# Kernel tuning notes

Measured on AMD Instinct MI355X. Metric: run time of the kernel, lower is better.

Reference implementation:

```python
import jax, jax.numpy as jnp
import numpy as np

H, W = 128, 128
FOCAL_X = FOCAL_Y = 128.0
NEAR = 0.3
N_GAUSS = 2048
EPS = 1e-4  # regularizer on 2D covariance diagonal


def q2r(q):
    """Quaternion (w,x,y,z) [N,4] -> rotation matrices [N,3,3]."""
    q = q / jnp.linalg.norm(q, axis=-1, keepdims=True)
    w, x, y, z = q[:, 0], q[:, 1], q[:, 2], q[:, 3]
    R = jnp.stack([
        1 - 2 * (y * y + z * z), 2 * (x * y - w * z), 2 * (x * z + w * y),
        2 * (x * y + w * z), 1 - 2 * (x * x + z * z), 2 * (y * z - w * x),
        2 * (x * z - w * y), 2 * (y * z + w * x), 1 - 2 * (x * x + y * y),
    ], axis=-1).reshape(-1, 3, 3)
    return R


def setup_inputs():
    key = jax.random.key(0)
    ks = jax.random.split(key, 6)
    # gaussians placed inside the camera frustum (camera looks along +z)
    xy = jax.random.uniform(ks[0], (N_GAUSS, 2), minval=-1.5, maxval=1.5)
    z = jax.random.uniform(ks[1], (N_GAUSS, 1), minval=2.0, maxval=6.0)
    pos = jnp.concatenate([xy * z / 4.0, z], axis=-1)
    rgb = jax.random.normal(ks[2], (N_GAUSS, 3))
    opa = jax.random.normal(ks[3], (N_GAUSS,))
    quat = jax.random.normal(ks[4], (N_GAUSS, 4))
    scale = jax.random.uniform(ks[5], (N_GAUSS, 3), minval=0.01, maxval=0.05)
    ang = 0.05  # small camera rotation about y
    rot = jnp.array([[np.cos(ang), 0.0, np.sin(ang)],
                     [0.0, 1.0, 0.0],
                     [-np.sin(ang), 0.0, np.cos(ang)]], dtype=jnp.float32)
    tran = jnp.array([0.0, 0.0, 0.1], dtype=jnp.float32)
    return {"pos": pos, "rgb": rgb, "opa": opa, "quat": quat,
            "scale": scale, "rot": rot, "tran": tran}


def _forward(pos, rgb, opa, quat, scale, rot, tran):
    # ---- project: world -> camera -> image space (Gaussian3ds.project) ----
    pos_cam = pos @ rot.T + tran                       # [N,3]
    x, y, z = pos_cam[:, 0], pos_cam[:, 1], pos_cam[:, 2]
    r = jnp.linalg.norm(pos_cam, axis=-1)              # depth = ||p_cam||
    u, v = x / z, y / z                                # normalized image coords
    zero = jnp.zeros_like(z)
    # jacobian of (x/z, y/z, ||p||) wrt camera coords (jacobian_torch)
    J = jnp.stack([1.0 / z, zero, -x / (z * z),
                   zero, 1.0 / z, -y / (z * z),
                   x / r, y / r, z / r], axis=-1).reshape(-1, 3, 3)
    # 3D covariance: R S S^T R^T with abs scale activation
    Rm = q2r(quat)
    s = jnp.abs(scale) + 1e-4
    RS = Rm * s[:, None, :]                            # R @ diag(s)
    cov3d = jnp.einsum('nij,nkj->nik', RS, RS)
    JW = jnp.einsum('nij,jk->nik', J, rot)
    cov2d = jnp.einsum('nij,njk,nlk->nil', JW, cov3d, JW)[:, :2, :2]
    a = cov2d[:, 0, 0] + EPS
    b = cov2d[:, 0, 1]
    c = cov2d[:, 1, 1] + EPS
    det = a * c - b * b
    ia, ib, ic = c / det, -b / det, a / det            # inverse 2x2 cov entries
    rgb_s = jax.nn.sigmoid(rgb)
    opa_s = jax.nn.sigmoid(opa)
    # ---- global front-to-back depth sort ----
    order = jnp.argsort(r)
    u, v = u[order], v[order]
    ia, ib, ic = ia[order], ib[order], ic[order]
    opa_s, zs = opa_s[order], z[order]
    rgb_s = rgb_s[order]
    # ---- alpha composite over all pixels (tiles merged -> dense) ----
    px = (jnp.arange(W) - W / 2 + 0.5) / FOCAL_X
    py = (jnp.arange(H) - H / 2 + 0.5) / FOCAL_Y
    yy, xx = jnp.meshgrid(py, px, indexing='ij')
    pxf, pyf = xx.reshape(-1), yy.reshape(-1)          # [P]
    dx = pxf[:, None] - u[None, :]                     # [P,N]
    dy = pyf[:, None] - v[None, :]
    power = -0.5 * (ia * dx * dx + 2.0 * ib * dx * dy + ic * dy * dy)
    alpha = jnp.clip(opa_s * jnp.exp(power), 0.0, 0.99)
    alpha = alpha * (zs > NEAR)                        # near-plane cull as mask
    T = jnp.cumprod(1.0 - alpha, axis=1)
    T_excl = jnp.concatenate([jnp.ones((T.shape[0], 1), T.dtype), T[:, :-1]], axis=1)
    img = (T_excl * alpha) @ rgb_s                     # [P,3]
    return img.reshape(H, W, 3)


def reference(pos, rgb, opa, quat, scale, rot, tran):
    return _forward(pos, rgb, opa, quat, scale, rot, tran)
```

## Files before the change

### kernel.cpp

```cpp
#include <hip/hip_runtime.h>
#include <hip/hip_bf16.h>

#define NG     2048
#define HW     128
#define NPIX   (HW*HW)
#define SEG    16
#define CHUNK  (NG/SEG)
#define NEARZ  0.3f
#define GEPS   1e-4f
#define LOG2E  1.4426950408889634f

__device__ float4   g_ga_s[NG];
__device__ float4   g_gb_s[NG];
__device__ float    g_cb_s[NG];
__device__ unsigned g_bb_s[NG];

__device__ __forceinline__ float sigm(float x) { return 1.0f / (1.0f + __expf(-x)); }

__device__ __forceinline__ bool detect_f32(const void* rot) {
    return ((const unsigned short*)rot)[1] != 0;
}
__device__ __forceinline__ float ld(const void* p, int idx, bool f32) {
    if (f32) return ((const float*)p)[idx];
    return __bfloat162float(((const __hip_bfloat16*)p)[idx]);
}

__global__ __launch_bounds__(256)
void prep_sort_kernel(const void* __restrict__ pos,
                      const void* __restrict__ rgb,
                      const void* __restrict__ opa,
                      const void* __restrict__ quat,
                      const void* __restrict__ scale,
                      const void* __restrict__ rot,
                      const void* __restrict__ tran)
{
    __shared__ float rs[NG];
    __shared__ int   srank[16];

    int tid = threadIdx.x;
    bool f32 = detect_f32(rot);

    float R[9], T3[3];
    #pragma unroll
    for (int k = 0; k < 9; k++) R[k] = ld(rot, k, f32);
    #pragma unroll
    for (int k = 0; k < 3; k++) T3[k] = ld(tran, k, f32);

    #pragma unroll
    for (int k = 0; k < NG / 256; k++) {
        int j = tid + k * 256;
        float p0 = ld(pos, j*3+0, f32), p1 = ld(pos, j*3+1, f32), p2 = ld(pos, j*3+2, f32);
        float x = R[0]*p0 + R[1]*p1 + R[2]*p2 + T3[0];
        float y = R[3]*p0 + R[4]*p1 + R[5]*p2 + T3[1];
        float z = R[6]*p0 + R[7]*p1 + R[8]*p2 + T3[2];
        rs[j] = sqrtf(x*x + y*y + z*z);
    }
    __syncthreads();

    int g      = blockIdx.x * 16 + (tid >> 4);
    int lane16 = tid & 15;
    float ri = rs[g];
    int rank = 0;
    int jbase = lane16 * CHUNK;
    #pragma unroll 4
    for (int jj = 0; jj < CHUNK; jj++) {
        int j = jbase + ((jj + 2 * lane16) & (CHUNK - 1));
        float rj = rs[j];
        rank += (rj < ri) || (rj == ri && j < g);
    }
    #pragma unroll
    for (int d = 1; d < 16; d <<= 1) rank += __shfl_xor(rank, d);
    if (lane16 == 0) srank[tid >> 4] = rank;
    __syncthreads();

    if (tid < 16) {
        int i  = blockIdx.x * 16 + tid;
        int rk = srank[tid];

        float p0 = ld(pos, i*3+0, f32), p1 = ld(pos, i*3+1, f32), p2 = ld(pos, i*3+2, f32);
        float x = R[0]*p0 + R[1]*p1 + R[2]*p2 + T3[0];
        float y = R[3]*p0 + R[4]*p1 + R[5]*p2 + T3[1];
        float z = R[6]*p0 + R[7]*p1 + R[8]*p2 + T3[2];
        float iz = 1.0f / z;
        float u = x * iz, v = y * iz;

        float qw = ld(quat, i*4+0, f32), qx = ld(quat, i*4+1, f32);
        float qy = ld(quat, i*4+2, f32), qz = ld(quat, i*4+3, f32);
        float qn = 1.0f / sqrtf(qw*qw + qx*qx + qy*qy + qz*qz);
        qw *= qn; qx *= qn; qy *= qn; qz *= qn;
        float Rm[3][3];
        Rm[0][0] = 1.0f - 2.0f*(qy*qy + qz*qz);
        Rm[0][1] = 2.0f*(qx*qy - qw*qz);
        Rm[0][2] = 2.0f*(qx*qz + qw*qy);
        Rm[1][0] = 2.0f*(qx*qy + qw*qz);
        Rm[1][1] = 1.0f - 2.0f*(qx*qx + qz*qz);
        Rm[1][2] = 2.0f*(qy*qz - qw*qx);
        Rm[2][0] = 2.0f*(qx*qz - qw*qy);
        Rm[2][1] = 2.0f*(qy*qz + qw*qx);
        Rm[2][2] = 1.0f - 2.0f*(qx*qx + qy*qy);

        float s[3];
        #pragma unroll
        for (int k = 0; k < 3; k++) s[k] = fabsf(ld(scale, i*3+k, f32)) + 1e-4f;

        float RS[3][3];
        #pragma unroll
        for (int a = 0; a < 3; a++)
            #pragma unroll
            for (int b = 0; b < 3; b++) RS[a][b] = Rm[a][b] * s[b];
        float C3[3][3];
        #pragma unroll
        for (int a = 0; a < 3; a++)
            #pragma unroll
            for (int b = 0; b < 3; b++)
                C3[a][b] = RS[a][0]*RS[b][0] + RS[a][1]*RS[b][1] + RS[a][2]*RS[b][2];

        float nx = -x * iz * iz, ny = -y * iz * iz;
        float jw0[3], jw1[3];
        #pragma unroll
        for (int k = 0; k < 3; k++) {
            jw0[k] = iz * R[0*3+k] + nx * R[2*3+k];
            jw1[k] = iz * R[1*3+k] + ny * R[2*3+k];
        }
        float t0[3], t1[3];
        #pragma unroll
        for (int j = 0; j < 3; j++) {
            t0[j] = C3[j][0]*jw0[0] + C3[j][1]*jw0[1] + C3[j][2]*jw0[2];
            t1[j] = C3[j][0]*jw1[0] + C3[j][1]*jw1[1] + C3[j][2]*jw1[2];
        }
        float a = jw0[0]*t0[0] + jw0[1]*t0[1] + jw0[2]*t0[2] + GEPS;
        float b = jw0[0]*t1[0] + jw0[1]*t1[1] + jw0[2]*t1[2];
        float c = jw1[0]*t1[0] + jw1[1]*t1[1] + jw1[2]*t1[2] + GEPS;
        float det  = a*c - b*b;
        float idet = 1.0f / det;
        float Af = -0.5f * LOG2E * (c * idet);
        float Bf = -LOG2E * (-b * idet);
        float Cf = -0.5f * LOG2E * (a * idet);

        float om = (z > NEARZ) ? sigm(ld(opa, i, f32)) : 0.0f;
        float cr = sigm(ld(rgb, i*3+0, f32));
        float cg = sigm(ld(rgb, i*3+1, f32));
        float cb = sigm(ld(rgb, i*3+2, f32));

        float mid = 0.5f * (a + c);
        float lam = mid + sqrtf(fmaxf(mid*mid - det, 0.0f));
        float rad = 6.5f * sqrtf(lam) * 128.0f;
        float u_px = u * 128.0f + 63.5f;
        float v_px = v * 128.0f + 63.5f;
        unsigned bb = 0xFF00FF00u;
        if (om > 0.0f) {
            int ymn = (int)ceilf (v_px - rad);
            int ymx = (int)floorf(v_px + rad);
            int xmn = (int)ceilf (u_px - rad);
            int xmx = (int)floorf(u_px + rad);
            if (ymx >= 0 && ymn <= 127 && xmx >= 0 && xmn <= 127) {
                ymn = max(ymn, 0); ymx = min(ymx, 127);
                xmn = max(xmn, 0); xmx = min(xmx, 127);
                bb = (unsigned)((ymn << 24) | (ymx << 16) | (xmn << 8) | xmx);
            }
        }

        g_ga_s[rk] = make_float4(u, v, Af, Bf);
        g_gb_s[rk] = make_float4(Cf, om, cr, cg);
        g_cb_s[rk] = cb;
        g_bb_s[rk] = bb;
    }
}

__global__ __launch_bounds__(1024)
void raster_kernel(void* __restrict__ out, const void* __restrict__ rot)
{
    __shared__ float4 comb[SEG * 64];

    int tid  = threadIdx.x;
    int lane = tid & 63;
    int w    = __builtin_amdgcn_readfirstlane(tid >> 6);

    int pix = blockIdx.x * 64 + lane;
    int row = blockIdx.x >> 1;
    int x0  = (blockIdx.x & 1) * 64;
    int x1  = x0 + 63;
    int col = x0 + lane;
    float pxf = (col - 63.5f) * (1.0f / 128.0f);
    float pyf = (row - 63.5f) * (1.0f / 128.0f);

    float T = 1.0f, Cr = 0.0f, Cg = 0.0f, Cb = 0.0f;
    int base = w * CHUNK;

    #pragma unroll
    for (int c = 0; c < CHUNK / 64; c++) {
        int cbase = base + c * 64;
        unsigned bb = g_bb_s[cbase + lane];
        int ymn =  bb >> 24;
        int ymx = (bb >> 16) & 255;
        int xmn = (bb >>  8) & 255;
        int xmx =  bb        & 255;
        bool hit = (row >= ymn) & (row <= ymx) & (x1 >= xmn) & (x0 <= xmx);
        unsigned long long m = __ballot(hit);
        while (m) {
            int kk = __builtin_ctzll(m);
            m &= m - 1;
            int idx = cbase + kk;
            float4 a4 = g_ga_s[idx];
            float4 b4 = g_gb_s[idx];
            float  cc = g_cb_s[idx];
            float dx = pxf - a4.x;
            float dy = pyf - a4.y;
            float p  = (a4.z * dx + a4.w * dy) * dx;
            p = fmaf(b4.x * dy, dy, p);
            float alpha = fminf(b4.y * __builtin_amdgcn_exp2f(p), 0.99f);
            float wgt = T * alpha;
            Cr = fmaf(wgt, b4.z, Cr);
            Cg = fmaf(wgt, b4.w, Cg);
            Cb = fmaf(wgt, cc, Cb);
            T -= wgt;
        }
    }

    comb[w * 64 + lane] = make_float4(T, Cr, Cg, Cb);
    __syncthreads();

    if (tid < 64) {
        float Ta = 1.0f, Ra = 0.0f, Ga = 0.0f, Ba = 0.0f;
        #pragma unroll
        for (int s = 0; s < SEG; s++) {
            float4 c4 = comb[s * 64 + lane];
            Ra = fmaf(Ta, c4.y, Ra);
            Ga = fmaf(Ta, c4.z, Ga);
            Ba = fmaf(Ta, c4.w, Ba);
            Ta *= c4.x;
        }
        if (detect_f32(rot)) {
            float* o = (float*)out;
            o[pix*3 + 0] = Ra; o[pix*3 + 1] = Ga; o[pix*3 + 2] = Ba;
        } else {
            __hip_bfloat16* o = (__hip_bfloat16*)out;
            o[pix*3 + 0] = __float2bfloat16(Ra);
            o[pix*3 + 1] = __float2bfloat16(Ga);
            o[pix*3 + 2] = __float2bfloat16(Ba);
        }
    }
}

extern "C" void kernel_launch(void* const* d_in, const int* in_sizes, int n_in,
                              void* d_out, int out_size, void* d_ws, size_t ws_size,
                              hipStream_t stream)
{
    const void* pos   = d_in[0];
    const void* rgb   = d_in[1];
    const void* opa   = d_in[2];
    const void* quat  = d_in[3];
    const void* scale = d_in[4];
    const void* rot   = d_in[5];
    const void* tran  = d_in[6];

    prep_sort_kernel<<<NG/16, 256, 0, stream>>>(pos, rgb, opa, quat, scale, rot, tran);
    raster_kernel<<<NPIX/64, 1024, 0, stream>>>(d_out, rot);
}
```

Measured before the change: 90.17 us.

## Fuse prep/sort and raster into one cooperative kernel with grid sync

```diff
diff --git a/kernel.cpp b/kernel.cpp
--- a/kernel.cpp
+++ b/kernel.cpp
@@ -1,11 +1,15 @@
 #include <hip/hip_runtime.h>
 #include <hip/hip_bf16.h>
+#include <hip/hip_cooperative_groups.h>
+
+namespace cg = cooperative_groups;
 
 #define NG     2048
 #define HW     128
 #define NPIX   (HW*HW)
 #define SEG    16
 #define CHUNK  (NG/SEG)
+#define GPB    (NG/256)
 #define NEARZ  0.3f
 #define GEPS   1e-4f
 #define LOG2E  1.4426950408889634f
@@ -25,160 +29,112 @@
     return __bfloat162float(((const __hip_bfloat16*)p)[idx]);
 }
 
-__global__ __launch_bounds__(256)
-void prep_sort_kernel(const void* __restrict__ pos,
-                      const void* __restrict__ rgb,
-                      const void* __restrict__ opa,
-                      const void* __restrict__ quat,
-                      const void* __restrict__ scale,
-                      const void* __restrict__ rot,
-                      const void* __restrict__ tran)
-{
-    __shared__ float rs[NG];
-    __shared__ int   srank[16];
-
-    int tid = threadIdx.x;
-    bool f32 = detect_f32(rot);
-
-    float R[9], T3[3];
-    #pragma unroll
-    for (int k = 0; k < 9; k++) R[k] = ld(rot, k, f32);
-    #pragma unroll
-    for (int k = 0; k < 3; k++) T3[k] = ld(tran, k, f32);
-
-    #pragma unroll
-    for (int k = 0; k < NG / 256; k++) {
-        int j = tid + k * 256;
-        float p0 = ld(pos, j*3+0, f32), p1 = ld(pos, j*3+1, f32), p2 = ld(pos, j*3+2, f32);
-        float x = R[0]*p0 + R[1]*p1 + R[2]*p2 + T3[0];
-        float y = R[3]*p0 + R[4]*p1 + R[5]*p2 + T3[1];
-        float z = R[6]*p0 + R[7]*p1 + R[8]*p2 + T3[2];
-        rs[j] = sqrtf(x*x + y*y + z*z);
-    }
-    __syncthreads();
-
-    int g      = blockIdx.x * 16 + (tid >> 4);
-    int lane16 = tid & 15;
-    float ri = rs[g];
-    int rank = 0;
-    int jbase = lane16 * CHUNK;
-    #pragma unroll 4
-    for (int jj = 0; jj < CHUNK; jj++) {
-        int j = jbase + ((jj + 2 * lane16) & (CHUNK - 1));
-        float rj = rs[j];
-        rank += (rj < ri) || (rj == ri && j < g);
-    }
-    #pragma unroll
-    for (int d = 1; d < 16; d <<= 1) rank += __shfl_xor(rank, d);
-    if (lane16 == 0) srank[tid >> 4] = rank;
-    __syncthreads();
-
-    if (tid < 16) {
-        int i  = blockIdx.x * 16 + tid;
-        int rk = srank[tid];
-
-        float p0 = ld(pos, i*3+0, f32), p1 = ld(pos, i*3+1, f32), p2 = ld(pos, i*3+2, f32);
-        float x = R[0]*p0 + R[1]*p1 + R[2]*p2 + T3[0];
-        float y = R[3]*p0 + R[4]*p1 + R[5]*p2 + T3[1];
-        float z = R[6]*p0 + R[7]*p1 + R[8]*p2 + T3[2];
-        float iz = 1.0f / z;
-        float u = x * iz, v = y * iz;
-
-        float qw = ld(quat, i*4+0, f32), qx = ld(quat, i*4+1, f32);
-        float qy = ld(quat, i*4+2, f32), qz = ld(quat, i*4+3, f32);
-        float qn = 1.0f / sqrtf(qw*qw + qx*qx + qy*qy + qz*qz);
-        qw *= qn; qx *= qn; qy *= qn; qz *= qn;
-        float Rm[3][3];
-        Rm[0][0] = 1.0f - 2.0f*(qy*qy + qz*qz);
-        Rm[0][1] = 2.0f*(qx*qy - qw*qz);
-        Rm[0][2] = 2.0f*(qx*qz + qw*qy);
-        Rm[1][0] = 2.0f*(qx*qy + qw*qz);
-        Rm[1][1] = 1.0f - 2.0f*(qx*qx + qz*qz);
-        Rm[1][2] = 2.0f*(qy*qz - qw*qx);
-        Rm[2][0] = 2.0f*(qx*qz - qw*qy);
-        Rm[2][1] = 2.0f*(qy*qz + qw*qx);
-        Rm[2][2] = 1.0f - 2.0f*(qx*qx + qy*qy);
-
-        float s[3];
+
+__device__ __forceinline__ void prep_one(int i, int rk, bool f32,
+                                         const float* R, const float* T3,
+                                         const void* pos, const void* rgb,
+                                         const void* opa, const void* quat,
+                                         const void* scale)
+{
+    float p0 = ld(pos, i*3+0, f32), p1 = ld(pos, i*3+1, f32), p2 = ld(pos, i*3+2, f32);
+    float x = R[0]*p0 + R[1]*p1 + R[2]*p2 + T3[0];
+    float y = R[3]*p0 + R[4]*p1 + R[5]*p2 + T3[1];
+    float z = R[6]*p0 + R[7]*p1 + R[8]*p2 + T3[2];
+    float iz = 1.0f / z;
+    float u = x * iz, v = y * iz;
+
+    float qw = ld(quat, i*4+0, f32), qx = ld(quat, i*4+1, f32);
+    float qy = ld(quat, i*4+2, f32), qz = ld(quat, i*4+3, f32);
+    float qn = 1.0f / sqrtf(qw*qw + qx*qx + qy*qy + qz*qz);
+    qw *= qn; qx *= qn; qy *= qn; qz *= qn;
+    float Rm[3][3];
+    Rm[0][0] = 1.0f - 2.0f*(qy*qy + qz*qz);
+    Rm[0][1] = 2.0f*(qx*qy - qw*qz);
+    Rm[0][2] = 2.0f*(qx*qz + qw*qy);
+    Rm[1][0] = 2.0f*(qx*qy + qw*qz);
+    Rm[1][1] = 1.0f - 2.0f*(qx*qx + qz*qz);
+    Rm[1][2] = 2.0f*(qy*qz - qw*qx);
+    Rm[2][0] = 2.0f*(qx*qz - qw*qy);
+    Rm[2][1] = 2.0f*(qy*qz + qw*qx);
+    Rm[2][2] = 1.0f - 2.0f*(qx*qx + qy*qy);
+
+    float s[3];
+    #pragma unroll
+    for (int k = 0; k < 3; k++) s[k] = fabsf(ld(scale, i*3+k, f32)) + 1e-4f;
+
+    float RS[3][3];
+    #pragma unroll
+    for (int a = 0; a < 3; a++)
         #pragma unroll
-        for (int k = 0; k < 3; k++) s[k] = fabsf(ld(scale, i*3+k, f32)) + 1e-4f;
-
-        float RS[3][3];
+        for (int b = 0; b < 3; b++) RS[a][b] = Rm[a][b] * s[b];
+    float C3[3][3];
+    #pragma unroll
+    for (int a = 0; a < 3; a++)
         #pragma unroll
-        for (int a = 0; a < 3; a++)
-            #pragma unroll
-            for (int b = 0; b < 3; b++) RS[a][b] = Rm[a][b] * s[b];
-        float C3[3][3];
-        #pragma unroll
-        for (int a = 0; a < 3; a++)
-            #pragma unroll
-            for (int b = 0; b < 3; b++)
-                C3[a][b] = RS[a][0]*RS[b][0] + RS[a][1]*RS[b][1] + RS[a][2]*RS[b][2];
-
-        float nx = -x * iz * iz, ny = -y * iz * iz;
-        float jw0[3], jw1[3];
-        #pragma unroll
-        for (int k = 0; k < 3; k++) {
-            jw0[k] = iz * R[0*3+k] + nx * R[2*3+k];
-            jw1[k] = iz * R[1*3+k] + ny * R[2*3+k];
-        }
-        float t0[3], t1[3];
-        #pragma unroll
-        for (int j = 0; j < 3; j++) {
-            t0[j] = C3[j][0]*jw0[0] + C3[j][1]*jw0[1] + C3[j][2]*jw0[2];
-            t1[j] = C3[j][0]*jw1[0] + C3[j][1]*jw1[1] + C3[j][2]*jw1[2];
-        }
-        float a = jw0[0]*t0[0] + jw0[1]*t0[1] + jw0[2]*t0[2] + GEPS;
-        float b = jw0[0]*t1[0] + jw0[1]*t1[1] + jw0[2]*t1[2];
-        float c = jw1[0]*t1[0] + jw1[1]*t1[1] + jw1[2]*t1[2] + GEPS;
-        float det  = a*c - b*b;
-        float idet = 1.0f / det;
-        float Af = -0.5f * LOG2E * (c * idet);
-        float Bf = -LOG2E * (-b * idet);
-        float Cf = -0.5f * LOG2E * (a * idet);
-
-        float om = (z > NEARZ) ? sigm(ld(opa, i, f32)) : 0.0f;
-        float cr = sigm(ld(rgb, i*3+0, f32));
-        float cg = sigm(ld(rgb, i*3+1, f32));
-        float cb = sigm(ld(rgb, i*3+2, f32));
-
-        float mid = 0.5f * (a + c);
-        float lam = mid + sqrtf(fmaxf(mid*mid - det, 0.0f));
-        float rad = 6.5f * sqrtf(lam) * 128.0f;
-        float u_px = u * 128.0f + 63.5f;
-        float v_px = v * 128.0f + 63.5f;
-        unsigned bb = 0xFF00FF00u;
-        if (om > 0.0f) {
-            int ymn = (int)ceilf (v_px - rad);
-            int ymx = (int)floorf(v_px + rad);
-            int xmn = (int)ceilf (u_px - rad);
-            int xmx = (int)floorf(u_px + rad);
-            if (ymx >= 0 && ymn <= 127 && xmx >= 0 && xmn <= 127) {
-                ymn = max(ymn, 0); ymx = min(ymx, 127);
-                xmn = max(xmn, 0); xmx = min(xmx, 127);
-                bb = (unsigned)((ymn << 24) | (ymx << 16) | (xmn << 8) | xmx);
-            }
-        }
-
-        g_ga_s[rk] = make_float4(u, v, Af, Bf);
-        g_gb_s[rk] = make_float4(Cf, om, cr, cg);
-        g_cb_s[rk] = cb;
-        g_bb_s[rk] = bb;
-    }
-}
-
-__global__ __launch_bounds__(1024)
-void raster_kernel(void* __restrict__ out, const void* __restrict__ rot)
-{
-    __shared__ float4 comb[SEG * 64];
-
-    int tid  = threadIdx.x;
+        for (int b = 0; b < 3; b++)
+            C3[a][b] = RS[a][0]*RS[b][0] + RS[a][1]*RS[b][1] + RS[a][2]*RS[b][2];
+
+    float nx = -x * iz * iz, ny = -y * iz * iz;
+    float jw0[3], jw1[3];
+    #pragma unroll
+    for (int k = 0; k < 3; k++) {
+        jw0[k] = iz * R[0*3+k] + nx * R[2*3+k];
+        jw1[k] = iz * R[1*3+k] + ny * R[2*3+k];
+    }
+    float t0[3], t1[3];
+    #pragma unroll
+    for (int j = 0; j < 3; j++) {
+        t0[j] = C3[j][0]*jw0[0] + C3[j][1]*jw0[1] + C3[j][2]*jw0[2];
+        t1[j] = C3[j][0]*jw1[0] + C3[j][1]*jw1[1] + C3[j][2]*jw1[2];
+    }
+    float a = jw0[0]*t0[0] + jw0[1]*t0[1] + jw0[2]*t0[2] + GEPS;
+    float b = jw0[0]*t1[0] + jw0[1]*t1[1] + jw0[2]*t1[2];
+    float c = jw1[0]*t1[0] + jw1[1]*t1[1] + jw1[2]*t1[2] + GEPS;
+    float det  = a*c - b*b;
+    float idet = 1.0f / det;
+    float Af = -0.5f * LOG2E * (c * idet);
+    float Bf = -LOG2E * (-b * idet);
+    float Cf = -0.5f * LOG2E * (a * idet);
+
+    float om = (z > NEARZ) ? sigm(ld(opa, i, f32)) : 0.0f;
+    float cr = sigm(ld(rgb, i*3+0, f32));
+    float cg = sigm(ld(rgb, i*3+1, f32));
+    float cb = sigm(ld(rgb, i*3+2, f32));
+
+    float mid = 0.5f * (a + c);
+    float lam = mid + sqrtf(fmaxf(mid*mid - det, 0.0f));
+    float rad = 6.5f * sqrtf(lam) * 128.0f;
+    float u_px = u * 128.0f + 63.5f;
+    float v_px = v * 128.0f + 63.5f;
+    unsigned bb = 0xFF00FF00u;
+    if (om > 0.0f) {
+        int ymn = (int)ceilf (v_px - rad);
+        int ymx = (int)floorf(v_px + rad);
+        int xmn = (int)ceilf (u_px - rad);
+        int xmx = (int)floorf(u_px + rad);
+        if (ymx >= 0 && ymn <= 127 && xmx >= 0 && xmn <= 127) {
+            ymn = max(ymn, 0); ymx = min(ymx, 127);
+            xmn = max(xmn, 0); xmx = min(xmx, 127);
+            bb = (unsigned)((ymn << 24) | (ymx << 16) | (xmn << 8) | xmx);
+        }
+    }
+
+    g_ga_s[rk] = make_float4(u, v, Af, Bf);
+    g_gb_s[rk] = make_float4(Cf, om, cr, cg);
+    g_cb_s[rk] = cb;
+    g_bb_s[rk] = bb;
+}
+
+__device__ __forceinline__ void raster_body(int strip, int tid,
+                                            float4* comb,
+                                            void* out, bool f32)
+{
     int lane = tid & 63;
     int w    = __builtin_amdgcn_readfirstlane(tid >> 6);
 
-    int pix = blockIdx.x * 64 + lane;
-    int row = blockIdx.x >> 1;
-    int x0  = (blockIdx.x & 1) * 64;
+    int pix = strip * 64 + lane;
+    int row = strip >> 1;
+    int x0  = (strip & 1) * 64;
     int x1  = x0 + 63;
     int col = x0 + lane;
     float pxf = (col - 63.5f) * (1.0f / 128.0f);
@@ -230,7 +186,7 @@
             Ba = fmaf(Ta, c4.w, Ba);
             Ta *= c4.x;
         }
-        if (detect_f32(rot)) {
+        if (f32) {
             float* o = (float*)out;
             o[pix*3 + 0] = Ra; o[pix*3 + 1] = Ga; o[pix*3 + 2] = Ba;
         } else {
@@ -242,6 +198,130 @@
     }
 }
 
+__global__ __launch_bounds__(1024, 4)
+void splat_coop_kernel(void* __restrict__ out,
+                       const void* __restrict__ pos,
+                       const void* __restrict__ rgb,
+                       const void* __restrict__ opa,
+                       const void* __restrict__ quat,
+                       const void* __restrict__ scale,
+                       const void* __restrict__ rot,
+                       const void* __restrict__ tran)
+{
+    __shared__ float  rs[NG];
+    __shared__ int    srank[GPB];
+    __shared__ float4 comb[SEG * 64];
+
+    int tid = threadIdx.x;
+    bool f32 = detect_f32(rot);
+
+    float R[9], T3[3];
+    #pragma unroll
+    for (int k = 0; k < 9; k++) R[k] = ld(rot, k, f32);
+    #pragma unroll
+    for (int k = 0; k < 3; k++) T3[k] = ld(tran, k, f32);
+
+    #pragma unroll
+    for (int k = 0; k < NG / 1024; k++) {
+        int j = tid + k * 1024;
+        float p0 = ld(pos, j*3+0, f32), p1 = ld(pos, j*3+1, f32), p2 = ld(pos, j*3+2, f32);
+        float x = R[0]*p0 + R[1]*p1 + R[2]*p2 + T3[0];
+        float y = R[3]*p0 + R[4]*p1 + R[5]*p2 + T3[1];
+        float z = R[6]*p0 + R[7]*p1 + R[8]*p2 + T3[2];
+        rs[j] = sqrtf(x*x + y*y + z*z);
+    }
+    __syncthreads();
+
+    if (tid < GPB * 64) {
+        int g    = blockIdx.x * GPB + (tid >> 6);
+        int lane = tid & 63;
+        float ri = rs[g];
+        int rank = 0;
+        int jbase = lane * (NG / 64);
+        #pragma unroll 8
+        for (int jj = 0; jj < NG / 64; jj++) {
+            int j = jbase + ((jj + lane) & (NG / 64 - 1));
+            float rj = rs[j];
+            rank += (rj < ri) || (rj == ri && j < g);
+        }
+        #pragma unroll
+        for (int d = 1; d < 64; d <<= 1) rank += __shfl_xor(rank, d);
+        if (lane == 0) srank[tid >> 6] = rank;
+    }
+    __syncthreads();
+
+    if (tid < GPB) {
+        int i = blockIdx.x * GPB + tid;
+        prep_one(i, srank[tid], f32, R, T3, pos, rgb, opa, quat, scale);
+    }
+
+    __threadfence();
+    cg::this_grid().sync();
+
+    raster_body(blockIdx.x, tid, comb, out, f32);
+}
+
+__global__ __launch_bounds__(256)
+void prep_sort_kernel(const void* __restrict__ pos,
+                      const void* __restrict__ rgb,
+                      const void* __restrict__ opa,
+                      const void* __restrict__ quat,
+                      const void* __restrict__ scale,
+                      const void* __restrict__ rot,
+                      const void* __restrict__ tran)
+{
+    __shared__ float rs[NG];
+    __shared__ int   srank[16];
+
+    int tid = threadIdx.x;
+    bool f32 = detect_f32(rot);
+
+    float R[9], T3[3];
+    #pragma unroll
+    for (int k = 0; k < 9; k++) R[k] = ld(rot, k, f32);
+    #pragma unroll
+    for (int k = 0; k < 3; k++) T3[k] = ld(tran, k, f32);
+
+    #pragma unroll
+    for (int k = 0; k < NG / 256; k++) {
+        int j = tid + k * 256;
+        float p0 = ld(pos, j*3+0, f32), p1 = ld(pos, j*3+1, f32), p2 = ld(pos, j*3+2, f32);
+        float x = R[0]*p0 + R[1]*p1 + R[2]*p2 + T3[0];
+        float y = R[3]*p0 + R[4]*p1 + R[5]*p2 + T3[1];
+        float z = R[6]*p0 + R[7]*p1 + R[8]*p2 + T3[2];
+        rs[j] = sqrtf(x*x + y*y + z*z);
+    }
+    __syncthreads();
+
+    int g      = blockIdx.x * 16 + (tid >> 4);
+    int lane16 = tid & 15;
+    float ri = rs[g];
+    int rank = 0;
+    int jbase = lane16 * CHUNK;
+    #pragma unroll 4
+    for (int jj = 0; jj < CHUNK; jj++) {
+        int j = jbase + ((jj + 2 * lane16) & (CHUNK - 1));
+        float rj = rs[j];
+        rank += (rj < ri) || (rj == ri && j < g);
+    }
+    #pragma unroll
+    for (int d = 1; d < 16; d <<= 1) rank += __shfl_xor(rank, d);
+    if (lane16 == 0) srank[tid >> 4] = rank;
+    __syncthreads();
+
+    if (tid < 16) {
+        int i = blockIdx.x * 16 + tid;
+        prep_one(i, srank[tid], f32, R, T3, pos, rgb, opa, quat, scale);
+    }
+}
+
+__global__ __launch_bounds__(1024)
+void raster_kernel(void* __restrict__ out, const void* __restrict__ rot)
+{
+    __shared__ float4 comb[SEG * 64];
+    raster_body(blockIdx.x, threadIdx.x, comb, out, detect_f32(rot));
+}
+
 extern "C" void kernel_launch(void* const* d_in, const int* in_sizes, int n_in,
                               void* d_out, int out_size, void* d_ws, size_t ws_size,
                               hipStream_t stream)
@@ -253,7 +333,16 @@
     const void* scale = d_in[4];
     const void* rot   = d_in[5];
     const void* tran  = d_in[6];
-
-    prep_sort_kernel<<<NG/16, 256, 0, stream>>>(pos, rgb, opa, quat, scale, rot, tran);
-    raster_kernel<<<NPIX/64, 1024, 0, stream>>>(d_out, rot);
-}
+    void* out = d_out;
+
+    void* args[] = { &out, (void*)&pos, (void*)&rgb, (void*)&opa, (void*)&quat,
+                     (void*)&scale, (void*)&rot, (void*)&tran };
+    hipError_t err = hipLaunchCooperativeKernel(
+        reinterpret_cast<const void*>(splat_coop_kernel),
+        dim3(NPIX / 64), dim3(1024), args, 0, stream);
+
+    if (err != hipSuccess) {
+        prep_sort_kernel<<<NG/16, 256, 0, stream>>>(pos, rgb, opa, quat, scale, rot, tran);
+        raster_kernel<<<NPIX/64, 1024, 0, stream>>>(d_out, rot);
+    }
+}
```

Result: slower. 198.4 us (+120.0%).
